# Optimization experiments

Hardware: AMD Instinct MI355X
Metric: run time of the kernel (lower is better)

Reference implementation:

```python
import jax, jax.numpy as jnp
import numpy as np

N = 50000   # nodes
E = 800000  # edges
D = 128     # node feature dim
H = 128     # hidden channels
G = 500     # graphs
EPS = 1e-5


def setup_inputs() -> dict:
    key = jax.random.key(0)
    ks = jax.random.split(key, 12)
    s = 0.05
    inp = {
        'x': jax.random.normal(ks[0], (N, D), jnp.float32),
        'edge_index': jax.random.randint(ks[1], (2, E), 0, N, jnp.int64),
        'batch': jnp.sort(jax.random.randint(ks[2], (N,), 0, G, jnp.int64)),
        'W1': jax.random.normal(ks[3], (D, H), jnp.float32) * s,
        'b1': jnp.zeros((H,), jnp.float32),
        'g1': jnp.ones((H,), jnp.float32),
        'be1': jnp.zeros((H,), jnp.float32),
        'W2': jax.random.normal(ks[4], (H, H), jnp.float32) * s,
        'b2': jnp.zeros((H,), jnp.float32),
        'g2': jnp.ones((H,), jnp.float32),
        'be2': jnp.zeros((H,), jnp.float32),
        'W3': jax.random.normal(ks[5], (H, H), jnp.float32) * s,
        'b3': jnp.zeros((H,), jnp.float32),
        'g3': jnp.ones((H,), jnp.float32),
        'be3': jnp.zeros((H,), jnp.float32),
        'fcW1': jax.random.normal(ks[6], (H, H // 2), jnp.float32) * s,
        'fcb1': jnp.zeros((H // 2,), jnp.float32),
        'fcg1': jnp.ones((H // 2,), jnp.float32),
        'fcbe1': jnp.zeros((H // 2,), jnp.float32),
        'fcW2': jax.random.normal(ks[7], (H // 2, 1), jnp.float32) * s,
        'fcb2': jnp.zeros((1,), jnp.float32),
    }
    return inp


def _bn(h, g, b):
    # training-mode BatchNorm1d: batch stats, biased variance
    m = h.mean(0)
    v = jnp.mean((h - m) ** 2, 0)
    return g * (h - m) * jax.lax.rsqrt(v + EPS) + b


def reference(x, edge_index, batch, W1, b1, g1, be1, W2, b2, g2, be2,
              W3, b3, g3, be3, fcW1, fcb1, fcg1, fcbe1, fcW2, fcb2):
    # GCN normalization with self-loops: D^{-1/2}(A+I)D^{-1/2}
    loop = jnp.arange(N, dtype=edge_index.dtype)
    src = jnp.concatenate([edge_index[0], loop])
    dst = jnp.concatenate([edge_index[1], loop])
    deg = jax.ops.segment_sum(jnp.ones_like(dst, dtype=x.dtype), dst, N)
    dis = jax.lax.rsqrt(jnp.maximum(deg, 1.0))  # deg>=1 due to self loops
    norm = dis[src] * dis[dst]  # [E+N]

    def conv_bn_relu(h, W, b, g, be):
        h = h @ W                                   # [N,H]
        msg = h[src] * norm[:, None]                # gather + scale
        agg = jax.ops.segment_sum(msg, dst, N) + b  # scatter-add
        return jax.nn.relu(_bn(agg, g, be))

    h = conv_bn_relu(x, W1, b1, g1, be1)
    h = conv_bn_relu(h, W2, b2, g2, be2)
    h = conv_bn_relu(h, W3, b3, g3, be3)

    # global_mean_pool per graph
    cnt = jax.ops.segment_sum(jnp.ones((N,), h.dtype), batch, G)
    pooled = jax.ops.segment_sum(h, batch, G) / jnp.maximum(cnt, 1.0)[:, None]

    z = pooled @ fcW1 + fcb1
    z = jax.nn.relu(_bn(z, fcg1, fcbe1))
    return z @ fcW2 + fcb2  # [G,1]
```

## Files before the change

kernel.cpp:

```cpp
#include <hip/hip_runtime.h>

#define EPS 1e-5f
constexpr int HD = 128;
constexpr int FCD = 64;

typedef __attribute__((ext_vector_type(8))) short short8;
typedef __attribute__((ext_vector_type(4))) float floatx4;

__device__ inline ushort f2bf(float f){
  union{float f; unsigned u;} v; v.f = f;
  unsigned r = v.u + 0x7FFFu + ((v.u >> 16) & 1u);
  return (ushort)(r >> 16);
}
__device__ inline float bflo(unsigned u){ union{unsigned i; float f;} v; v.i = u << 16;        return v.f; }
__device__ inline float bfhi(unsigned u){ union{unsigned i; float f;} v; v.i = u & 0xFFFF0000u; return v.f; }
__device__ inline float bf2f(ushort u){ union{unsigned i; float f;} v; v.i = ((unsigned)u) << 16; return v.f; }


__global__ __launch_bounds__(256) void k_hist(const int* __restrict__ dst,
                                              int* __restrict__ bucketHist, int E){
  __shared__ int h[256];
  int t = threadIdx.x;
  h[t] = 0;
  __syncthreads();
  int base = blockIdx.x*4096;
  #pragma unroll
  for (int k = 0; k < 16; ++k){
    int e = base + k*256 + t;
    if (e < E) atomicAdd(&h[dst[e] >> 8], 1);
  }
  __syncthreads();
  if (h[t]) atomicAdd(&bucketHist[t], h[t]);
}

__global__ __launch_bounds__(256) void k_bscan(const int* __restrict__ bucketHist,
                                               int* __restrict__ bucketBase,
                                               int* __restrict__ bucketCursor){
  __shared__ int wt[4];
  int t = threadIdx.x, lane = t & 63, w = t >> 6;
  int v = bucketHist[t];
  int incl = v;
  #pragma unroll
  for (int o = 1; o < 64; o <<= 1){
    int x = __shfl_up(incl, o, 64);
    if (lane >= o) incl += x;
  }
  if (lane == 63) wt[w] = incl;
  __syncthreads();
  int woff = 0;
  for (int i = 0; i < w; ++i) woff += wt[i];
  int ex = woff + incl - v;
  bucketBase[t] = ex;
  bucketCursor[t] = ex;
}

__global__ __launch_bounds__(256) void k_bucket(const int* __restrict__ src,
                                                const int* __restrict__ dst,
                                                int* __restrict__ bucketCursor,
                                                int2* __restrict__ tmp, int E){
  __shared__ int h[256], ls[256], cur[256], gb[256];
  __shared__ int wt[4];
  __shared__ int2 staged[4096];
  __shared__ unsigned char bos[4096];
  int t = threadIdx.x, lane = t & 63, w = t >> 6;
  int base = blockIdx.x*4096;
  int2 ed[16]; int bk[16];
  h[t] = 0;
  __syncthreads();
  #pragma unroll
  for (int k = 0; k < 16; ++k){
    int e = base + k*256 + t;
    if (e < E){
      int s = src[e], d = dst[e];
      ed[k] = make_int2(s, d);
      bk[k] = d >> 8;
      atomicAdd(&h[bk[k]], 1);
    } else bk[k] = -1;
  }
  __syncthreads();
  int v = h[t];
  int incl = v;
  #pragma unroll
  for (int o = 1; o < 64; o <<= 1){
    int x = __shfl_up(incl, o, 64);
    if (lane >= o) incl += x;
  }
  if (lane == 63) wt[w] = incl;
  __syncthreads();
  int woff = 0;
  for (int i = 0; i < w; ++i) woff += wt[i];
  ls[t] = woff + incl - v;
  cur[t] = ls[t];
  if (v > 0) gb[t] = atomicAdd(&bucketCursor[t], v);
  __syncthreads();
  #pragma unroll
  for (int k = 0; k < 16; ++k){
    if (bk[k] >= 0){
      int lp = atomicAdd(&cur[bk[k]], 1);
      staged[lp] = ed[k];
      bos[lp] = (unsigned char)bk[k];
    }
  }
  __syncthreads();
  int nvalid = min(4096, E - base);
  #pragma unroll
  for (int k = 0; k < 16; ++k){
    int i = k*256 + t;
    if (i < nvalid){
      int b = bos[i];
      tmp[gb[b] + (i - ls[b])] = staged[i];
    }
  }
}

__global__ __launch_bounds__(256) void k_csr(const int2* __restrict__ tmp,
                                             const int* __restrict__ bucketHist,
                                             const int* __restrict__ bucketBase,
                                             int* __restrict__ rowptr,
                                             float* __restrict__ dis,
                                             int* __restrict__ csrc, int N){
  __shared__ int h[256], ls[256], cur[256];
  __shared__ int wt[4];
  __shared__ int stagedSrc[6144];
  int b = blockIdx.x, t = threadIdx.x, lane = t & 63, w = t >> 6;
  int ebase = bucketBase[b];
  int cnt = bucketHist[b];
  int node0 = b << 8;
  h[t] = 0;
  __syncthreads();
  for (int i = t; i < cnt; i += 256){
    int2 e = tmp[ebase + i];
    atomicAdd(&h[e.y - node0], 1);
  }
  __syncthreads();
  int v = h[t];
  int incl = v;
  #pragma unroll
  for (int o = 1; o < 64; o <<= 1){
    int x = __shfl_up(incl, o, 64);
    if (lane >= o) incl += x;
  }
  if (lane == 63) wt[w] = incl;
  __syncthreads();
  int woff = 0;
  for (int i = 0; i < w; ++i) woff += wt[i];
  int ex = woff + incl - v;
  ls[t] = ex; cur[t] = ex;
  int d = node0 + t;
  if (d < N){
    rowptr[d+1] = ebase + ex + v;
    dis[d] = rsqrtf((float)v + 1.0f);
  }
  if (b == 0 && t == 0) rowptr[0] = 0;
  __syncthreads();
  for (int i = t; i < cnt; i += 256){
    int2 e = tmp[ebase + i];
    int lp = atomicAdd(&cur[e.y - node0], 1);
    stagedSrc[lp] = e.x;
  }
  __syncthreads();
  for (int i = t; i < cnt; i += 256)
    csrc[ebase + i] = stagedSrc[i];
}

__global__ void k_prepW(const float* __restrict__ W1, const float* __restrict__ W2,
                        const float* __restrict__ W3, ushort* __restrict__ Wf){
  const float* Ws[3] = {W1, W2, W3};
  int l = blockIdx.y;
  int idx = blockIdx.x*256 + threadIdx.x;
  int k = idx >> 7, n = idx & 127;
  float w = Ws[l][idx];
  int kb = k >> 5, q = (k >> 3) & 3, j = k & 7;
  int nt = n >> 4, col = n & 15;
  Wf[(size_t)l*16384 + (((size_t)(kb*8 + nt)*64 + q*16 + col)*8 + j)] = f2bf(w);
}

template<int MODE>
__global__ __launch_bounds__(256) void k_gemm(const void* __restrict__ Av,
                                              const ushort* __restrict__ Wf,
                                              const float* __restrict__ sums,
                                              const float* __restrict__ g,
                                              const float* __restrict__ be,
                                              const float* __restrict__ dis,
                                              ushort* __restrict__ O, int n, float invN){
  __shared__ float aL[HD], bL[HD];
  int tid = threadIdx.x;
  if (MODE){
    if (tid < HD){
      float m = sums[tid]*invN;
      float var = fmaxf(sums[HD+tid]*invN - m*m, 0.f);
      float Ac = g[tid]*rsqrtf(var + EPS);
      aL[tid] = Ac; bL[tid] = be[tid] - m*Ac;
    }
    __syncthreads();
  }
  int lane = tid & 63, wave = tid >> 6;
  int quad = lane >> 4, r16 = lane & 15;
  int row = blockIdx.x*64 + wave*16 + r16;
  int rowc = min(row, n-1);
  floatx4 acc[8] = {};
  #pragma unroll
  for (int kb = 0; kb < 4; ++kb){
    int k0 = kb*32 + quad*8;
    short8 af;
    if (MODE){
      const ushort* Arow = (const ushort*)Av + (size_t)rowc*HD;
      short8 raw = *(const short8*)(Arow + k0);
      #pragma unroll
      for (int jj = 0; jj < 8; ++jj){
        float f = bf2f((ushort)raw[jj]);
        f = fmaxf(f*aL[k0+jj] + bL[k0+jj], 0.f);
        af[jj] = (short)f2bf(f);
      }
    } else {
      const float* Arow = (const float*)Av + (size_t)rowc*HD;
      float4 x0 = *(const float4*)(Arow + k0);
      float4 x1 = *(const float4*)(Arow + k0 + 4);
      af[0] = (short)f2bf(x0.x); af[1] = (short)f2bf(x0.y);
      af[2] = (short)f2bf(x0.z); af[3] = (short)f2bf(x0.w);
      af[4] = (short)f2bf(x1.x); af[5] = (short)f2bf(x1.y);
      af[6] = (short)f2bf(x1.z); af[7] = (short)f2bf(x1.w);
    }
    const ushort* wp = Wf + ((size_t)(kb*8)*64 + lane)*8;
    #pragma unroll
    for (int nt = 0; nt < 8; ++nt){
      short8 bf = *(const short8*)(wp + (size_t)nt*64*8);
      acc[nt] = __builtin_amdgcn_mfma_f32_16x16x32_bf16(af, bf, acc[nt], 0, 0, 0);
    }
  }
  int rbase = blockIdx.x*64 + wave*16 + quad*4;
  float ds[4];
  #pragma unroll
  for (int r = 0; r < 4; ++r) ds[r] = dis[min(rbase + r, n-1)];
  #pragma unroll
  for (int nt = 0; nt < 8; ++nt){
    #pragma unroll
    for (int r = 0; r < 4; ++r){
      int rr = rbase + r;
      if (rr < n) O[(size_t)rr*HD + nt*16 + r16] = f2bf(acc[nt][r]*ds[r]);
    }
  }
}

__global__ __launch_bounds__(256) void k_gather(const ushort* __restrict__ hw,
                                                const int* __restrict__ rowptr,
                                                const int* __restrict__ csrc,
                                                const float* __restrict__ dis,
                                                ushort* __restrict__ agg,
                                                float* __restrict__ scratch,
                                                float* __restrict__ sums, int N){
  __shared__ float2 sm[4][HD];
  if (blockIdx.x == 0) sums[threadIdx.x] = 0.f;
  int grp = threadIdx.x >> 4, j = threadIdx.x & 15;
  int wave = threadIdx.x >> 6, lane = threadIdx.x & 63;
  int i = blockIdx.x*16 + grp;
  bool valid = (i < N);
  int ic = valid ? i : N-1;
  uint4 q = ((const uint4*)(hw + (size_t)ic*HD))[j];
  float a[8];
  a[0] = bflo(q.x); a[1] = bfhi(q.x);
  a[2] = bflo(q.y); a[3] = bfhi(q.y);
  a[4] = bflo(q.z); a[5] = bfhi(q.z);
  a[6] = bflo(q.w); a[7] = bfhi(q.w);
  int e = rowptr[ic], e1 = rowptr[ic+1];
  #define ADD8(Q) \
    a[0] += bflo(Q.x); a[1] += bfhi(Q.x); \
    a[2] += bflo(Q.y); a[3] += bfhi(Q.y); \
    a[4] += bflo(Q.z); a[5] += bfhi(Q.z); \
    a[6] += bflo(Q.w); a[7] += bfhi(Q.w);
  while (e < e1 && (e & 3)){
    uint4 qq = ((const uint4*)(hw + (size_t)csrc[e]*HD))[j];
    ADD8(qq);
    e++;
  }
  int4 c0, c1;
  if (e + 8 <= e1){
    c0 = *(const int4*)&csrc[e];
    c1 = *(const int4*)&csrc[e+4];
  }
  while (e + 8 <= e1){
    int en = e + 8;
    int4 n0, n1;
    if (en + 8 <= e1){
      n0 = *(const int4*)&csrc[en];
      n1 = *(const int4*)&csrc[en+4];
    }
    uint4 q0 = ((const uint4*)(hw + (size_t)c0.x*HD))[j];
    uint4 q1 = ((const uint4*)(hw + (size_t)c0.y*HD))[j];
    uint4 q2 = ((const uint4*)(hw + (size_t)c0.z*HD))[j];
    uint4 q3 = ((const uint4*)(hw + (size_t)c0.w*HD))[j];
    uint4 q4 = ((const uint4*)(hw + (size_t)c1.x*HD))[j];
    uint4 q5 = ((const uint4*)(hw + (size_t)c1.y*HD))[j];
    uint4 q6 = ((const uint4*)(hw + (size_t)c1.z*HD))[j];
    uint4 q7 = ((const uint4*)(hw + (size_t)c1.w*HD))[j];
    ADD8(q0); ADD8(q1); ADD8(q2); ADD8(q3);
    ADD8(q4); ADD8(q5); ADD8(q6); ADD8(q7);
    c0 = n0; c1 = n1; e = en;
  }
  if (e + 4 <= e1){
    int4 tt = *(const int4*)&csrc[e];
    uint4 q0 = ((const uint4*)(hw + (size_t)tt.x*HD))[j];
    uint4 q1 = ((const uint4*)(hw + (size_t)tt.y*HD))[j];
    uint4 q2 = ((const uint4*)(hw + (size_t)tt.z*HD))[j];
    uint4 q3 = ((const uint4*)(hw + (size_t)tt.w*HD))[j];
    ADD8(q0); ADD8(q1); ADD8(q2); ADD8(q3);
    e += 4;
  }
  for (; e < e1; ++e){
    uint4 qq = ((const uint4*)(hw + (size_t)csrc[e]*HD))[j];
    ADD8(qq);
  }
  #undef ADD8
  float sc = dis[ic];
  #pragma unroll
  for (int k = 0; k < 8; ++k) a[k] *= sc;
  if (valid){
    uint4 o;
    o.x = (unsigned)f2bf(a[0]) | ((unsigned)f2bf(a[1]) << 16);
    o.y = (unsigned)f2bf(a[2]) | ((unsigned)f2bf(a[3]) << 16);
    o.z = (unsigned)f2bf(a[4]) | ((unsigned)f2bf(a[5]) << 16);
    o.w = (unsigned)f2bf(a[6]) | ((unsigned)f2bf(a[7]) << 16);
    ((uint4*)(agg + (size_t)i*HD))[j] = o;
  }
  float z = valid ? 1.f : 0.f;
  #pragma unroll
  for (int k = 0; k < 8; ++k){
    float s = a[k]*z, qq = a[k]*a[k]*z;
    s  += __shfl_xor(s, 16);  s  += __shfl_xor(s, 32);
    qq += __shfl_xor(qq, 16); qq += __shfl_xor(qq, 32);
    if (lane < 16) sm[wave][lane*8 + k] = make_float2(s, qq);
  }
  __syncthreads();
  int t = threadIdx.x;
  if (t < HD){
    float2 r0 = sm[0][t], r1 = sm[1][t], r2 = sm[2][t], r3 = sm[3][t];
    scratch[(size_t)blockIdx.x*256 + t]      = r0.x + r1.x + r2.x + r3.x;
    scratch[(size_t)blockIdx.x*256 + HD + t] = r0.y + r1.y + r2.y + r3.y;
  }
}

__global__ __launch_bounds__(256) void k_reduce(const float* __restrict__ scratch,
                                                float* __restrict__ sums, int R){
  int t = threadIdx.x;
  float acc = 0.f;
  for (int r = blockIdx.x; r < R; r += gridDim.x)
    acc += scratch[(size_t)r*256 + t];
  atomicAdd(&sums[t], acc);
}


__global__ __launch_bounds__(128) void k_pool(const ushort* __restrict__ h,
                                              const int* __restrict__ batch,
                                              const float* __restrict__ sums,
                                              const float* __restrict__ g,
                                              const float* __restrict__ be,
                                              float* __restrict__ pooled,
                                              float* __restrict__ cntf, int N, float invN){
  int c = threadIdx.x;
  float m = sums[c]*invN;
  float var = fmaxf(sums[HD+c]*invN - m*m, 0.f);
  float a = g[c]*rsqrtf(var + EPS);
  float b = be[c] - m*a;
  int start = blockIdx.x * 32;
  if (start >= N) return;
  int end = min(start + 32, N);
  int cur = batch[start];
  float acc = 0.f; int run = 0;
  for (int i = start; i < end; ++i){
    int bb = batch[i];
    if (bb != cur){
      atomicAdd(&pooled[(size_t)cur*HD + c], acc);
      if (c == 0) atomicAdd(&cntf[cur], (float)run);
      acc = 0.f; run = 0; cur = bb;
    }
    acc += fmaxf(bf2f(h[(size_t)i*HD + c])*a + b, 0.f);
    run++;
  }
  atomicAdd(&pooled[(size_t)cur*HD + c], acc);
  if (c == 0) atomicAdd(&cntf[cur], (float)run);
}


__global__ __launch_bounds__(64) void k_fc1(const float* __restrict__ pooled,
                                            const float* __restrict__ cntf,
                                            const float* __restrict__ W,
                                            const float* __restrict__ b,
                                            float* __restrict__ z,
                                            float* __restrict__ sums2, int G){
  int g = blockIdx.x, j = threadIdx.x;
  if (g == 0){ sums2[j] = 0.f; sums2[FCD + j] = 0.f; }
  float inv = 1.0f / fmaxf(cntf[g], 1.0f);
  float acc = 0.f;
  for (int k = 0; k < HD; ++k)
    acc += pooled[(size_t)g*HD + k] * W[k*FCD + j];
  z[(size_t)g*FCD + j] = acc * inv + b[j];
}

__global__ __launch_bounds__(64) void k_stats2(const float* __restrict__ z,
                                               float* __restrict__ sums2, int G){
  int c = threadIdx.x;
  float s = 0.f, q = 0.f;
  for (int i = blockIdx.x; i < G; i += gridDim.x){
    float v = z[(size_t)i*FCD + c]; s += v; q += v*v;
  }
  atomicAdd(&sums2[c], s);
  atomicAdd(&sums2[FCD + c], q);
}

__global__ __launch_bounds__(64) void k_final(const float* __restrict__ z,
                                              const float* __restrict__ sums2,
                                              const float* __restrict__ g,
                                              const float* __restrict__ be,
                                              const float* __restrict__ w2,
                                              const float* __restrict__ b2,
                                              float* __restrict__ out, int G, float invG){
  int gg = blockIdx.x, c = threadIdx.x;
  float m = sums2[c]*invG;
  float var = fmaxf(sums2[FCD+c]*invG - m*m, 0.f);
  float A = g[c]*rsqrtf(var + EPS);
  float B = be[c] - m*A;
  float v = fmaxf(z[(size_t)gg*FCD + c]*A + B, 0.f) * w2[c];
  #pragma unroll
  for (int o = 32; o > 0; o >>= 1) v += __shfl_down(v, o, 64);
  if (c == 0) out[gg] = v + b2[0];
}


extern "C" void kernel_launch(void* const* d_in, const int* in_sizes, int n_in,
                              void* d_out, int out_size, void* d_ws, size_t ws_size,
                              hipStream_t stream){
  const float* x    = (const float*)d_in[0];
  const int*   ei   = (const int*)d_in[1];
  const int*   batch= (const int*)d_in[2];
  const float* W1 = (const float*)d_in[3];
  const float* g1 = (const float*)d_in[5];
  const float* be1= (const float*)d_in[6];
  const float* W2 = (const float*)d_in[7];
  const float* g2 = (const float*)d_in[9];
  const float* be2= (const float*)d_in[10];
  const float* W3 = (const float*)d_in[11];
  const float* g3 = (const float*)d_in[13];
  const float* be3= (const float*)d_in[14];
  const float* fcW1 = (const float*)d_in[15];
  const float* fcb1 = (const float*)d_in[16];
  const float* fcg1 = (const float*)d_in[17];
  const float* fcbe1= (const float*)d_in[18];
  const float* fcW2 = (const float*)d_in[19];
  const float* fcb2 = (const float*)d_in[20];
  float* out = (float*)d_out;

  const int N = in_sizes[0] / HD;
  const int E = in_sizes[1] / 2;
  const int G = out_size;

  const int* esrc = ei;
  const int* edst = ei + E;

  char* p = (char*)d_ws;
  auto alloc = [&](size_t bytes)->void*{
    void* r = (void*)p; p += (bytes + 255) & ~(size_t)255; return r;
  };
  int gatherBlocks = (N + 15)/16;
  int nEB = (E + 4095)/4096;
  int NB  = (N + 255)/256;
  int*    bucketHist  = (int*) alloc(256*4);
  int*    bucketBase  = (int*) alloc(256*4);
  int*    bucketCursor= (int*) alloc(256*4);
  int2*   tmp    = (int2*)  alloc((size_t)E*8);
  int*    rowptr = (int*)   alloc((size_t)(N+1)*4);
  int*    csrc   = (int*)   alloc((size_t)E*4);
  float*  dis    = (float*) alloc((size_t)N*4);
  ushort* HWb    = (ushort*)alloc((size_t)N*HD*2);
  ushort* AGG    = (ushort*)alloc((size_t)N*HD*2);
  ushort* Wf     = (ushort*)alloc((size_t)3*HD*HD*2);
  float*  sums   = (float*) alloc(2*HD*4);
  float*  scratch= (float*) alloc((size_t)gatherBlocks*256*4);
  float*  pooled = (float*) alloc(((size_t)G*HD + G)*4);
  float*  cntf   = pooled + (size_t)G*HD;
  float*  zbuf   = (float*) alloc((size_t)G*FCD*4);
  float*  sums2  = (float*) alloc(2*FCD*4);

  float invN = 1.0f/(float)N, invG = 1.0f/(float)G;

  hipMemsetAsync(bucketHist, 0, 256*4, stream);
  k_hist  <<<nEB, 256, 0, stream>>>(edst, bucketHist, E);
  k_bscan <<<1, 256, 0, stream>>>(bucketHist, bucketBase, bucketCursor);
  k_bucket<<<nEB, 256, 0, stream>>>(esrc, edst, bucketCursor, tmp, E);
  k_csr   <<<NB, 256, 0, stream>>>(tmp, bucketHist, bucketBase, rowptr, dis, csrc, N);
  k_prepW <<<dim3(64,3), 256, 0, stream>>>(W1, W2, W3, Wf);

  int gemmBlocks = (N + 63)/64;

  k_gemm<0> <<<gemmBlocks, 256, 0, stream>>>(x,   Wf,         nullptr, nullptr, nullptr, dis, HWb, N, invN);
  k_gather  <<<gatherBlocks, 256, 0, stream>>>(HWb, rowptr, csrc, dis, AGG, scratch, sums, N);
  k_reduce  <<<64, 256, 0, stream>>>(scratch, sums, gatherBlocks);
  k_gemm<1> <<<gemmBlocks, 256, 0, stream>>>(AGG, Wf + 16384, sums, g1, be1, dis, HWb, N, invN);
  k_gather  <<<gatherBlocks, 256, 0, stream>>>(HWb, rowptr, csrc, dis, AGG, scratch, sums, N);
  k_reduce  <<<64, 256, 0, stream>>>(scratch, sums, gatherBlocks);
  k_gemm<1> <<<gemmBlocks, 256, 0, stream>>>(AGG, Wf + 32768, sums, g2, be2, dis, HWb, N, invN);
  k_gather  <<<gatherBlocks, 256, 0, stream>>>(HWb, rowptr, csrc, dis, AGG, scratch, sums, N);
  k_reduce  <<<64, 256, 0, stream>>>(scratch, sums, gatherBlocks);

  hipMemsetAsync(pooled, 0, ((size_t)G*HD + G)*4, stream);
  k_pool  <<<(N+31)/32, 128, 0, stream>>>(AGG, batch, sums, g3, be3, pooled, cntf, N, invN);
  k_fc1   <<<G, FCD, 0, stream>>>(pooled, cntf, fcW1, fcb1, zbuf, sums2, G);
  k_stats2<<<64, FCD, 0, stream>>>(zbuf, sums2, G);
  k_final <<<G, FCD, 0, stream>>>(zbuf, sums2, fcg1, fcbe1, fcW2, fcb2, out, G, invG);
}
```

Before: 360.0 us.

## Merge setup kernels, drop reduce passes, and pool per graph via batch pointers

Folds histogram, weight prep, and a new batch-pointer build into one setup kernel. Replaces the per-layer scratch+reduce step with direct atomic accumulation of BN statistics into per-layer pre-zeroed buffers. Pooling becomes one block per graph using segment pointers with vectorized loads, which removes the pooled memset and count atomics. BN stats for the FC layer are accumulated inside fc1, removing k_stats2. The goal is fewer launches and less global traffic, at the cost of many float atomics and nondeterministic summation order.

Result: slower. 487.6 us (+35.5%).

```diff
diff --git a/kernel.cpp b/kernel.cpp
--- a/kernel.cpp
+++ b/kernel.cpp
@@ -16,21 +16,48 @@
 __device__ inline float bfhi(unsigned u){ union{unsigned i; float f;} v; v.i = u & 0xFFFF0000u; return v.f; }
 __device__ inline float bf2f(ushort u){ union{unsigned i; float f;} v; v.i = ((unsigned)u) << 16; return v.f; }
 
-
-__global__ __launch_bounds__(256) void k_hist(const int* __restrict__ dst,
-                                              int* __restrict__ bucketHist, int E){
+__global__ __launch_bounds__(256) void k_setup(const int* __restrict__ dst,
+                                               int* __restrict__ bucketHist, int E, int nEB,
+                                               const int* __restrict__ batch,
+                                               int* __restrict__ batchPtr, int N, int G, int nBB,
+                                               const float* __restrict__ W1,
+                                               const float* __restrict__ W2,
+                                               const float* __restrict__ W3,
+                                               ushort* __restrict__ Wf){
   __shared__ int h[256];
   int t = threadIdx.x;
-  h[t] = 0;
-  __syncthreads();
-  int base = blockIdx.x*4096;
-  #pragma unroll
-  for (int k = 0; k < 16; ++k){
-    int e = base + k*256 + t;
-    if (e < E) atomicAdd(&h[dst[e] >> 8], 1);
-  }
-  __syncthreads();
-  if (h[t]) atomicAdd(&bucketHist[t], h[t]);
+  int b = blockIdx.x;
+  if (b < nEB){
+    h[t] = 0;
+    __syncthreads();
+    int base = b*4096;
+    #pragma unroll
+    for (int k = 0; k < 16; ++k){
+      int e = base + k*256 + t;
+      if (e < E) atomicAdd(&h[dst[e] >> 8], 1);
+    }
+    __syncthreads();
+    if (h[t]) atomicAdd(&bucketHist[t], h[t]);
+  } else if (b < nEB + nBB){
+    int i = (b - nEB)*256 + t;
+    if (i < N){
+      int bb = batch[i];
+      int prev = (i == 0) ? -1 : batch[i-1];
+      for (int g = prev + 1; g <= bb; ++g) batchPtr[g] = i;
+      if (i == N-1)
+        for (int g = bb + 1; g <= G; ++g) batchPtr[g] = N;
+    }
+  } else {
+    int idx4 = b - nEB - nBB;
+    int l = idx4 >> 6;
+    int idx = (idx4 & 63)*256 + t;
+    const float* Ws = (l == 0) ? W1 : (l == 1) ? W2 : W3;
+    int k = idx >> 7, n = idx & 127;
+    float w = Ws[idx];
+    int kb = k >> 5, q = (k >> 3) & 3, jj = k & 7;
+    int nt = n >> 4, col = n & 15;
+    Wf[(size_t)l*16384 + (((size_t)(kb*8 + nt)*64 + q*16 + col)*8 + jj)] = f2bf(w);
+  }
 }
 
 __global__ __launch_bounds__(256) void k_bscan(const int* __restrict__ bucketHist,
@@ -161,18 +188,6 @@
   __syncthreads();
   for (int i = t; i < cnt; i += 256)
     csrc[ebase + i] = stagedSrc[i];
-}
-
-__global__ void k_prepW(const float* __restrict__ W1, const float* __restrict__ W2,
-                        const float* __restrict__ W3, ushort* __restrict__ Wf){
-  const float* Ws[3] = {W1, W2, W3};
-  int l = blockIdx.y;
-  int idx = blockIdx.x*256 + threadIdx.x;
-  int k = idx >> 7, n = idx & 127;
-  float w = Ws[l][idx];
-  int kb = k >> 5, q = (k >> 3) & 3, j = k & 7;
-  int nt = n >> 4, col = n & 15;
-  Wf[(size_t)l*16384 + (((size_t)(kb*8 + nt)*64 + q*16 + col)*8 + j)] = f2bf(w);
 }
 
 template<int MODE>
@@ -247,10 +262,8 @@
                                                 const int* __restrict__ csrc,
                                                 const float* __restrict__ dis,
                                                 ushort* __restrict__ agg,
-                                                float* __restrict__ scratch,
-                                                float* __restrict__ sums, int N){
+                                                float* __restrict__ sumsOut, int N){
   __shared__ float2 sm[4][HD];
-  if (blockIdx.x == 0) sums[threadIdx.x] = 0.f;
   int grp = threadIdx.x >> 4, j = threadIdx.x & 15;
   int wave = threadIdx.x >> 6, lane = threadIdx.x & 63;
   int i = blockIdx.x*16 + grp;
@@ -334,77 +347,74 @@
   int t = threadIdx.x;
   if (t < HD){
     float2 r0 = sm[0][t], r1 = sm[1][t], r2 = sm[2][t], r3 = sm[3][t];
-    scratch[(size_t)blockIdx.x*256 + t]      = r0.x + r1.x + r2.x + r3.x;
-    scratch[(size_t)blockIdx.x*256 + HD + t] = r0.y + r1.y + r2.y + r3.y;
-  }
-}
-
-__global__ __launch_bounds__(256) void k_reduce(const float* __restrict__ scratch,
-                                                float* __restrict__ sums, int R){
-  int t = threadIdx.x;
-  float acc = 0.f;
-  for (int r = blockIdx.x; r < R; r += gridDim.x)
-    acc += scratch[(size_t)r*256 + t];
-  atomicAdd(&sums[t], acc);
-}
-
-
-__global__ __launch_bounds__(128) void k_pool(const ushort* __restrict__ h,
-                                              const int* __restrict__ batch,
+    atomicAdd(&sumsOut[t],      r0.x + r1.x + r2.x + r3.x);
+    atomicAdd(&sumsOut[HD + t], r0.y + r1.y + r2.y + r3.y);
+  }
+}
+
+__global__ __launch_bounds__(256) void k_pool(const ushort* __restrict__ h,
+                                              const int* __restrict__ batchPtr,
                                               const float* __restrict__ sums,
-                                              const float* __restrict__ g,
+                                              const float* __restrict__ gw,
                                               const float* __restrict__ be,
-                                              float* __restrict__ pooled,
-                                              float* __restrict__ cntf, int N, float invN){
-  int c = threadIdx.x;
-  float m = sums[c]*invN;
-  float var = fmaxf(sums[HD+c]*invN - m*m, 0.f);
-  float a = g[c]*rsqrtf(var + EPS);
-  float b = be[c] - m*a;
-  int start = blockIdx.x * 32;
-  if (start >= N) return;
-  int end = min(start + 32, N);
-  int cur = batch[start];
-  float acc = 0.f; int run = 0;
-  for (int i = start; i < end; ++i){
-    int bb = batch[i];
-    if (bb != cur){
-      atomicAdd(&pooled[(size_t)cur*HD + c], acc);
-      if (c == 0) atomicAdd(&cntf[cur], (float)run);
-      acc = 0.f; run = 0; cur = bb;
-    }
-    acc += fmaxf(bf2f(h[(size_t)i*HD + c])*a + b, 0.f);
-    run++;
-  }
-  atomicAdd(&pooled[(size_t)cur*HD + c], acc);
-  if (c == 0) atomicAdd(&cntf[cur], (float)run);
+                                              float* __restrict__ pooled, float invN){
+  __shared__ float sm[4][HD];
+  int g = blockIdx.x;
+  int start = batchPtr[g], end = batchPtr[g+1];
+  int tid = threadIdx.x;
+  int j = tid & 15, r = tid >> 4;
+  int wave = tid >> 6, lane = tid & 63;
+  float aC[8], bC[8];
+  #pragma unroll
+  for (int k = 0; k < 8; ++k){
+    int c = j*8 + k;
+    float m = sums[c]*invN;
+    float var = fmaxf(sums[HD+c]*invN - m*m, 0.f);
+    float A = gw[c]*rsqrtf(var + EPS);
+    aC[k] = A; bC[k] = be[c] - m*A;
+  }
+  float acc[8] = {};
+  for (int i = start + r; i < end; i += 16){
+    uint4 q = ((const uint4*)(h + (size_t)i*HD))[j];
+    acc[0] += fmaxf(bflo(q.x)*aC[0] + bC[0], 0.f);
+    acc[1] += fmaxf(bfhi(q.x)*aC[1] + bC[1], 0.f);
+    acc[2] += fmaxf(bflo(q.y)*aC[2] + bC[2], 0.f);
+    acc[3] += fmaxf(bfhi(q.y)*aC[3] + bC[3], 0.f);
+    acc[4] += fmaxf(bflo(q.z)*aC[4] + bC[4], 0.f);
+    acc[5] += fmaxf(bfhi(q.z)*aC[5] + bC[5], 0.f);
+    acc[6] += fmaxf(bflo(q.w)*aC[6] + bC[6], 0.f);
+    acc[7] += fmaxf(bfhi(q.w)*aC[7] + bC[7], 0.f);
+  }
+  #pragma unroll
+  for (int k = 0; k < 8; ++k){
+    float s = acc[k];
+    s += __shfl_xor(s, 16); s += __shfl_xor(s, 32);
+    if (lane < 16) sm[wave][lane*8 + k] = s;
+  }
+  __syncthreads();
+  if (tid < HD){
+    float tot = sm[0][tid] + sm[1][tid] + sm[2][tid] + sm[3][tid];
+    float inv = 1.0f / (float)max(end - start, 1);
+    pooled[(size_t)g*HD + tid] = tot * inv;
+  }
 }
 
 
 __global__ __launch_bounds__(64) void k_fc1(const float* __restrict__ pooled,
-                                            const float* __restrict__ cntf,
                                             const float* __restrict__ W,
                                             const float* __restrict__ b,
                                             float* __restrict__ z,
                                             float* __restrict__ sums2, int G){
   int g = blockIdx.x, j = threadIdx.x;
-  if (g == 0){ sums2[j] = 0.f; sums2[FCD + j] = 0.f; }
-  float inv = 1.0f / fmaxf(cntf[g], 1.0f);
+  const float* pr = pooled + (size_t)g*HD;
   float acc = 0.f;
+  #pragma unroll 8
   for (int k = 0; k < HD; ++k)
-    acc += pooled[(size_t)g*HD + k] * W[k*FCD + j];
-  z[(size_t)g*FCD + j] = acc * inv + b[j];
-}
-
-__global__ __launch_bounds__(64) void k_stats2(const float* __restrict__ z,
-                                               float* __restrict__ sums2, int G){
-  int c = threadIdx.x;
-  float s = 0.f, q = 0.f;
-  for (int i = blockIdx.x; i < G; i += gridDim.x){
-    float v = z[(size_t)i*FCD + c]; s += v; q += v*v;
-  }
-  atomicAdd(&sums2[c], s);
-  atomicAdd(&sums2[FCD + c], q);
+    acc += pr[k] * W[k*FCD + j];
+  float zv = acc + b[j];
+  z[(size_t)g*FCD + j] = zv;
+  atomicAdd(&sums2[j], zv);
+  atomicAdd(&sums2[FCD + j], zv*zv);
 }
 
 __global__ __launch_bounds__(64) void k_final(const float* __restrict__ z,
@@ -462,10 +472,16 @@
   };
   int gatherBlocks = (N + 15)/16;
   int nEB = (E + 4095)/4096;
+  int nBB = (N + 255)/256;
   int NB  = (N + 255)/256;
-  int*    bucketHist  = (int*) alloc(256*4);
+
+  size_t zeroBytes = 256*4 + 3*2*HD*4 + 2*FCD*4;
+  int*    bucketHist  = (int*) alloc(zeroBytes);
+  float*  sumsL  = (float*)(bucketHist + 256);
+  float*  sums2  = sumsL + 3*2*HD;
   int*    bucketBase  = (int*) alloc(256*4);
   int*    bucketCursor= (int*) alloc(256*4);
+  int*    batchPtr = (int*) alloc((size_t)(G+1)*4);
   int2*   tmp    = (int2*)  alloc((size_t)E*8);
   int*    rowptr = (int*)   alloc((size_t)(N+1)*4);
   int*    csrc   = (int*)   alloc((size_t)E*4);
@@ -473,37 +489,28 @@
   ushort* HWb    = (ushort*)alloc((size_t)N*HD*2);
   ushort* AGG    = (ushort*)alloc((size_t)N*HD*2);
   ushort* Wf     = (ushort*)alloc((size_t)3*HD*HD*2);
-  float*  sums   = (float*) alloc(2*HD*4);
-  float*  scratch= (float*) alloc((size_t)gatherBlocks*256*4);
-  float*  pooled = (float*) alloc(((size_t)G*HD + G)*4);
-  float*  cntf   = pooled + (size_t)G*HD;
+  float*  pooled = (float*) alloc((size_t)G*HD*4);
   float*  zbuf   = (float*) alloc((size_t)G*FCD*4);
-  float*  sums2  = (float*) alloc(2*FCD*4);
 
   float invN = 1.0f/(float)N, invG = 1.0f/(float)G;
 
-  hipMemsetAsync(bucketHist, 0, 256*4, stream);
-  k_hist  <<<nEB, 256, 0, stream>>>(edst, bucketHist, E);
+  hipMemsetAsync(bucketHist, 0, zeroBytes, stream);
+  k_setup <<<nEB + nBB + 3*(HD*HD/256), 256, 0, stream>>>(
+      edst, bucketHist, E, nEB, batch, batchPtr, N, G, nBB, W1, W2, W3, Wf);
   k_bscan <<<1, 256, 0, stream>>>(bucketHist, bucketBase, bucketCursor);
   k_bucket<<<nEB, 256, 0, stream>>>(esrc, edst, bucketCursor, tmp, E);
   k_csr   <<<NB, 256, 0, stream>>>(tmp, bucketHist, bucketBase, rowptr, dis, csrc, N);
-  k_prepW <<<dim3(64,3), 256, 0, stream>>>(W1, W2, W3, Wf);
 
   int gemmBlocks = (N + 63)/64;
 
   k_gemm<0> <<<gemmBlocks, 256, 0, stream>>>(x,   Wf,         nullptr, nullptr, nullptr, dis, HWb, N, invN);
-  k_gather  <<<gatherBlocks, 256, 0, stream>>>(HWb, rowptr, csrc, dis, AGG, scratch, sums, N);
-  k_reduce  <<<64, 256, 0, stream>>>(scratch, sums, gatherBlocks);
-  k_gemm<1> <<<gemmBlocks, 256, 0, stream>>>(AGG, Wf + 16384, sums, g1, be1, dis, HWb, N, invN);
-  k_gather  <<<gatherBlocks, 256, 0, stream>>>(HWb, rowptr, csrc, dis, AGG, scratch, sums, N);
-  k_reduce  <<<64, 256, 0, stream>>>(scratch, sums, gatherBlocks);
-  k_gemm<1> <<<gemmBlocks, 256, 0, stream>>>(AGG, Wf + 32768, sums, g2, be2, dis, HWb, N, invN);
-  k_gather  <<<gatherBlocks, 256, 0, stream>>>(HWb, rowptr, csrc, dis, AGG, scratch, sums, N);
-  k_reduce  <<<64, 256, 0, stream>>>(scratch, sums, gatherBlocks);
-
-  hipMemsetAsync(pooled, 0, ((size_t)G*HD + G)*4, stream);
-  k_pool  <<<(N+31)/32, 128, 0, stream>>>(AGG, batch, sums, g3, be3, pooled, cntf, N, invN);
-  k_fc1   <<<G, FCD, 0, stream>>>(pooled, cntf, fcW1, fcb1, zbuf, sums2, G);
-  k_stats2<<<64, FCD, 0, stream>>>(zbuf, sums2, G);
+  k_gather  <<<gatherBlocks, 256, 0, stream>>>(HWb, rowptr, csrc, dis, AGG, sumsL, N);
+  k_gemm<1> <<<gemmBlocks, 256, 0, stream>>>(AGG, Wf + 16384, sumsL, g1, be1, dis, HWb, N, invN);
+  k_gather  <<<gatherBlocks, 256, 0, stream>>>(HWb, rowptr, csrc, dis, AGG, sumsL + 2*HD, N);
+  k_gemm<1> <<<gemmBlocks, 256, 0, stream>>>(AGG, Wf + 32768, sumsL + 2*HD, g2, be2, dis, HWb, N, invN);
+  k_gather  <<<gatherBlocks, 256, 0, stream>>>(HWb, rowptr, csrc, dis, AGG, sumsL + 4*HD, N);
+
+  k_pool  <<<G, 256, 0, stream>>>(AGG, batchPtr, sumsL + 4*HD, g3, be3, pooled, invN);
+  k_fc1   <<<G, FCD, 0, stream>>>(pooled, fcW1, fcb1, zbuf, sums2, G);
   k_final <<<G, FCD, 0, stream>>>(zbuf, sums2, fcg1, fcbe1, fcW2, fcb2, out, G, invG);
 }
```
